# Kernel tuning notes

Hardware: AMD Instinct MI355X
Metric: run time of the kernel (lower is better)

Reference implementation:

```python
import jax, jax.numpy as jnp
import numpy as np

V, E, H, B, T = 50000, 300, 512, 256, 64
D_OUT = 3
EPS = 1e-5


def setup_inputs() -> dict:
    key = jax.random.key(0)
    ks = jax.random.split(key, 16)
    s = lambda k, shape: (jax.random.normal(k, shape, jnp.float32) * 0.05)
    return {
        "premise": jax.random.randint(ks[0], (T, B), 0, V),
        "hypothesis": jax.random.randint(ks[1], (T, B), 0, V),
        "embed": s(ks[2], (V, E)),
        "W_ih": s(ks[3], (4 * H, E)),
        "W_hh": s(ks[4], (4 * H, H)),
        "b_ih": s(ks[5], (4 * H,)),
        "b_hh": s(ks[6], (4 * H,)),
        "bn0_g": jnp.ones((4 * H,), jnp.float32),
        "bn0_b": jnp.zeros((4 * H,), jnp.float32),
        "W0": s(ks[7], (4 * H, 4 * H)),
        "b0": s(ks[8], (4 * H,)),
        "bn1_g": jnp.ones((4 * H,), jnp.float32),
        "bn1_b": jnp.zeros((4 * H,), jnp.float32),
        "W1": s(ks[9], (4 * H, 4 * H)),
        "b1": s(ks[10], (4 * H,)),
        "bno_g": jnp.ones((4 * H,), jnp.float32),
        "bno_b": jnp.zeros((4 * H,), jnp.float32),
        "Wo": s(ks[11], (D_OUT, 4 * H)),
        "bo": s(ks[12], (D_OUT,)),
    }


def _lstm_final_h(xs, W_ih, W_hh, bias):
    # xs: [T, N, E]; shared-weight LSTMCell scan, returns final hidden [N, H]
    x_proj = jnp.einsum('tne,ge->tng', xs, W_ih) + bias  # hoist input GEMM out of the recurrence
    n = xs.shape[1]
    h0 = jnp.zeros((n, H), xs.dtype)

    def step(carry, xg):
        h, c = carry
        gates = xg + h @ W_hh.T
        i, f, g, o = jnp.split(gates, 4, axis=-1)  # torch LSTMCell gate order
        c = jax.nn.sigmoid(f) * c + jax.nn.sigmoid(i) * jnp.tanh(g)
        h = jax.nn.sigmoid(o) * jnp.tanh(c)
        return (h, c), None

    (h, _), _ = jax.lax.scan(step, (h0, h0), x_proj)
    return h


def _bn(x, g, b):
    # BatchNorm1d in training mode: biased batch stats
    mu = x.mean(0)
    var = x.var(0)
    return (x - mu) * jax.lax.rsqrt(var + EPS) * g + b


def reference(premise, hypothesis, embed, W_ih, W_hh, b_ih, b_hh,
              bn0_g, bn0_b, W0, b0, bn1_g, bn1_b, W1, b1,
              bno_g, bno_b, Wo, bo):
    p = embed[premise]      # [T, B, E]
    hyp = embed[hypothesis]  # [T, B, E]
    combined = jnp.concatenate([p, hyp], axis=1)  # [T, 2B, E]
    bias = b_ih + b_hh
    h_fw = _lstm_final_h(combined, W_ih, W_hh, bias)          # forward direction
    h_bw = _lstm_final_h(combined[::-1], W_ih, W_hh, bias)    # backward direction (shared cell)
    feat = jnp.concatenate([h_fw[:B], h_bw[:B], h_fw[B:], h_bw[B:]], axis=1)  # [B, 4H]
    x = jax.nn.relu(_bn(feat, bn0_g, bn0_b) @ W0.T + b0)
    x = jax.nn.relu(_bn(x, bn1_g, bn1_b) @ W1.T + b1)
    return _bn(x, bno_g, bno_b) @ Wo.T + bo  # [B, d_out]
```

## Files before the change

### kernel.cpp

```cpp
#include <hip/hip_runtime.h>
#include <hip/hip_bf16.h>


typedef __attribute__((ext_vector_type(8))) short bf16x8;
typedef __attribute__((ext_vector_type(4))) float f32x4;
typedef __attribute__((ext_vector_type(4))) unsigned int u32x4;

#define DEVI __device__ __forceinline__

template<int N> struct IC { static constexpr int v = N; };

DEVI void async16(const void* g, void* l) {
  __builtin_amdgcn_global_load_lds((const __attribute__((address_space(1))) void*)g,
                                   (__attribute__((address_space(3))) void*)l,
                                   16, 0, 0);
}
DEVI void async16_coh(const void* g, void* l) {
  __builtin_amdgcn_global_load_lds((const __attribute__((address_space(1))) void*)g,
                                   (__attribute__((address_space(3))) void*)l,
                                   16, 0, 17);
}
DEVI void store16_coh(void* addr, u32x4 v) {
  asm volatile("global_store_dwordx4 %0, %1, off sc0 sc1" ::"v"(addr), "v"(v) : "memory");
}
DEVI bf16x8 load16_pin(const void* addr) {
  bf16x8 r;
  asm volatile("global_load_dwordx4 %0, %1, off" : "=v"(r) : "v"(addr) : "memory");
  return r;
}
template<int N> DEVI void vmwait_barrier() {
  asm volatile("s_waitcnt vmcnt(%0)" ::"i"(N) : "memory");
  __builtin_amdgcn_s_barrier();
  __builtin_amdgcn_sched_barrier(0);
}
DEVI float sigmf_(float x) { return 1.f / (1.f + __expf(-x)); }
DEVI float tanhf_(float x) {
  float a = __expf(-2.f * fabsf(x));
  float t = (1.f - a) / (1.f + a);
  return copysignf(t, x);
}
DEVI __hip_bfloat16 f2b(float x) { return __float2bfloat16(x); }
DEVI float b2f(__hip_bfloat16 x) { return __bfloat162float(x); }

__global__ void cvt_f32_bf16(const float* __restrict__ src,
                             __hip_bfloat16* __restrict__ dst, int n4) {
  int i = blockIdx.x * 256 + threadIdx.x;
  int stride = gridDim.x * 256;
  for (; i < n4; i += stride) {
    float4 v = ((const float4*)src)[i];
    union { __hip_bfloat16 h[4]; uint2 u; } o;
    o.h[0] = f2b(v.x); o.h[1] = f2b(v.y); o.h[2] = f2b(v.z); o.h[3] = f2b(v.w);
    ((uint2*)dst)[i] = o.u;
  }
}

__global__ void pack_wih(const float* __restrict__ W_ih,
                         const float* __restrict__ b_ih,
                         const float* __restrict__ b_hh,
                         __hip_bfloat16* __restrict__ WihP,
                         float* __restrict__ biasL) {
  int tid = blockIdx.x * 256 + threadIdx.x;
  int stride = gridDim.x * 256;
  for (int i = tid; i < 2048 * 320; i += stride) {
    int r = i / 320, c = i - r * 320;
    WihP[i] = (c < 300) ? f2b(W_ih[r * 300 + c]) : f2b(0.f);
  }
  if (tid < 2048) biasL[tid] = b_ih[tid] + b_hh[tid];
}

__global__ void gather_kernel(const int* __restrict__ prem, const int* __restrict__ hyp,
                              const float* __restrict__ embed,
                              __hip_bfloat16* __restrict__ Ain) {
  int row = blockIdx.x * 4 + (threadIdx.x >> 6);
  int lane = threadIdx.x & 63;
  int tt = row >> 9, n = row & 511;
  int tok = (n < 256) ? prem[tt * 256 + n] : hyp[tt * 256 + (n - 256)];
  const float4* e4 = (const float4*)(embed + (size_t)tok * 300);
  uint2* d2 = (uint2*)(Ain + (size_t)row * 320);
  for (int j = lane; j < 75; j += 64) {
    float4 v = e4[j];
    union { __hip_bfloat16 h[4]; uint2 u; } o;
    o.h[0] = f2b(v.x); o.h[1] = f2b(v.y); o.h[2] = f2b(v.z); o.h[3] = f2b(v.w);
    d2[j] = o.u;
  }
  for (int j = 75 + lane; j < 80; j += 64) d2[j] = make_uint2(0u, 0u);
}

template<int BM, int EPI>
__global__ __launch_bounds__(256)
void gemm_pipe(const __hip_bfloat16* __restrict__ A,
               const __hip_bfloat16* __restrict__ Bn,
               const float* __restrict__ bias,
               void* __restrict__ Cout, int K, int ldc) {
  constexpr int BK = 64;
  constexpr int ABYT = BM * BK * 2;
  constexpr int BBYT = 128 * BK * 2;
  constexpr int APW = BM / 32;
  constexpr int IFL = APW + 4;
  constexpr int WM = BM / 2, MT = WM / 16;
  __shared__ alignas(16) char smem[2 * ABYT + 2 * BBYT];

  const int tid = threadIdx.x, lane = tid & 63, wid = tid >> 6;
  const int wrow = wid >> 1, wcol = wid & 1;
  const int m0 = blockIdx.x * BM, n0 = blockIdx.y * 128;
  const int l8 = lane & 7, ld8 = lane >> 3;
  const int swz = (l8 ^ ld8) * 8;

  const __hip_bfloat16* Abase = A + (size_t)m0 * K;
  const __hip_bfloat16* Bbase = Bn + (size_t)n0 * K;

  f32x4 acc[MT][4];
#pragma unroll
  for (int i = 0; i < MT; ++i)
#pragma unroll
    for (int j = 0; j < 4; ++j) acc[i][j] = {0.f, 0.f, 0.f, 0.f};

  auto stage = [&](int buf, int kt) {
    const __hip_bfloat16* as = Abase + kt * BK + swz;
    char* ad = smem + buf * ABYT;
#pragma unroll
    for (int s = 0; s < APW; ++s) {
      int iss = wid * APW + s;
      async16(as + (size_t)(iss * 8 + ld8) * K, ad + iss * 1024);
    }
    const __hip_bfloat16* bs = Bbase + kt * BK + swz;
    char* bd = smem + 2 * ABYT + buf * BBYT;
#pragma unroll
    for (int s = 0; s < 4; ++s) {
      int iss = wid * 4 + s;
      async16(bs + (size_t)(iss * 8 + ld8) * K, bd + iss * 1024);
    }
  };

  const int nk = K / BK;
  stage(0, 0);
  for (int kt = 0; kt < nk; ++kt) {
    if (kt + 1 < nk) {
      stage((kt + 1) & 1, kt + 1);
      vmwait_barrier<IFL>();
    } else {
      vmwait_barrier<0>();
    }
    const __hip_bfloat16* ab = (const __hip_bfloat16*)(smem + (kt & 1) * ABYT);
    const __hip_bfloat16* bb = (const __hip_bfloat16*)(smem + 2 * ABYT + (kt & 1) * BBYT);
#pragma unroll
    for (int kk = 0; kk < BK; kk += 32) {
      bf16x8 af[MT], bf[4];
#pragma unroll
      for (int i = 0; i < MT; ++i) {
        int r = wrow * WM + i * 16 + (lane & 15);
        af[i] = *(const bf16x8*)&ab[r * BK + ((kk + (lane >> 4) * 8) ^ ((r & 7) * 8))];
      }
#pragma unroll
      for (int j = 0; j < 4; ++j) {
        int r = wcol * 64 + j * 16 + (lane & 15);
        bf[j] = *(const bf16x8*)&bb[r * BK + ((kk + (lane >> 4) * 8) ^ ((r & 7) * 8))];
      }
#pragma unroll
      for (int i = 0; i < MT; ++i)
#pragma unroll
        for (int j = 0; j < 4; ++j)
          acc[i][j] = __builtin_amdgcn_mfma_f32_16x16x32_bf16(af[i], bf[j], acc[i][j], 0, 0, 0);
    }
    __builtin_amdgcn_s_barrier();
  }

  if (EPI == 2) {
#pragma unroll
    for (int i = 0; i < MT; ++i)
#pragma unroll
      for (int j = 0; j < 4; ++j) {
        union { __hip_bfloat16 h[4]; uint2 u; } o;
#pragma unroll
        for (int rr = 0; rr < 4; ++rr) o.h[rr] = f2b(acc[i][j][rr]);
        size_t slot = (((size_t)blockIdx.x * 16 + blockIdx.y) * 4 + wid) * 16 + i * 4 + j;
        *(uint2*)((char*)Cout + slot * 512 + lane * 8) = o.u;
      }
    return;
  }

  __syncthreads();
  float* Csm = (float*)smem;
#pragma unroll
  for (int i = 0; i < MT; ++i)
#pragma unroll
    for (int j = 0; j < 4; ++j)
#pragma unroll
      for (int rr = 0; rr < 4; ++rr) {
        int row = wrow * WM + i * 16 + (lane >> 4) * 4 + rr;
        int col = wcol * 64 + j * 16 + (lane & 15);
        Csm[row * 128 + (col ^ ((row & 7) << 2))] = acc[i][j][rr];
      }
  __syncthreads();
#pragma unroll
  for (int it = 0; it < BM / 16; ++it) {
    int idx = it * 256 + tid;
    int row = idx >> 4;
    int cb = (idx & 15) * 8;
    int sw = (row & 7) << 2;
    float4 v0 = *(const float4*)&Csm[row * 128 + (cb ^ sw)];
    float4 v1 = *(const float4*)&Csm[row * 128 + ((cb + 4) ^ sw)];
    float4 b0 = *(const float4*)&bias[n0 + cb];
    float4 b1 = *(const float4*)&bias[n0 + cb + 4];
    v0.x = fmaxf(v0.x + b0.x, 0.f); v0.y = fmaxf(v0.y + b0.y, 0.f);
    v0.z = fmaxf(v0.z + b0.z, 0.f); v0.w = fmaxf(v0.w + b0.w, 0.f);
    v1.x = fmaxf(v1.x + b1.x, 0.f); v1.y = fmaxf(v1.y + b1.y, 0.f);
    v1.z = fmaxf(v1.z + b1.z, 0.f); v1.w = fmaxf(v1.w + b1.w, 0.f);
    size_t base = (size_t)(m0 + row) * ldc + n0 + cb;
    *(float4*)&((float*)Cout)[base] = v0;
    *(float4*)&((float*)Cout)[base + 4] = v1;
  }
}

__global__ __launch_bounds__(256, 1)
void lstm_persist(const __hip_bfloat16* __restrict__ xp,
                  const __hip_bfloat16* __restrict__ Whh,
                  const float* __restrict__ biasL,
                  __hip_bfloat16* __restrict__ hA,
                  __hip_bfloat16* __restrict__ hB,
                  int* __restrict__ ctr) {
  extern __shared__ char smem[];
  const int tid = threadIdx.x, lane = tid & 63, wid = tid >> 6;
  const int bid = blockIdx.x;
  const int grp = (bid & 7) | ((bid >> 7) << 3);
  const int jt = (bid >> 3) & 15;
  const int m0 = grp * 64;
  const int l8 = lane & 7, ld8 = lane >> 3;
  const int swz = (l8 ^ ld8) * 8;

  bf16x8 w[2][16];
  for (int h = 0; h < 2; ++h) {
#pragma unroll
    for (int kt = 0; kt < 8; ++kt)
#pragma unroll
      for (int s = 0; s < 2; ++s) {
        int iss = wid * 2 + s;
        int r = h * 64 + iss * 8 + ld8;
        int g = jt * 32 + (r >> 5) * 512 + (r & 31);
        async16(Whh + (size_t)g * 512 + kt * 64 + swz,
                smem + kt * 8192 + iss * 1024);
      }
    asm volatile("s_waitcnt vmcnt(0)" ::: "memory");
    __builtin_amdgcn_s_barrier();
    __builtin_amdgcn_sched_barrier(0);
    if ((wid >> 1) == h) {
      const __hip_bfloat16* wb = (const __hip_bfloat16*)smem;
      const int lw = wid & 1;
#pragma unroll
      for (int j = 0; j < 2; ++j)
#pragma unroll
        for (int ka = 0; ka < 16; ++ka) {
          int r = lw * 32 + j * 16 + (lane & 15);
          int kt = ka >> 1, kk = (ka & 1) * 32;
          w[j][ka] = *(const bf16x8*)&wb[kt * 4096 + r * 64 +
                                         ((kk + (lane >> 4) * 8) ^ ((r & 7) * 8))];
        }
    }
    __syncthreads();
  }

  const int jsel = (lane >> 5) & 1;
  const int qx = (lane >> 3) & 3;
  const int lane_x = (lane & 31) * 2;
  const int lane_lo = (lane & 7) * 2;
  const int col5b = jsel * 16 + lane_lo;
  const int wrx = grp & 1;
  const int wcx = (jt & 3) >> 1;
  const int widx = wrx * 2 + wcx;
  const int jx = (jt & 1) * 2 + jsel;
  const int ntb = jt >> 2;

  float bias_[4][2];
#pragma unroll
  for (int g = 0; g < 4; ++g)
#pragma unroll
    for (int cc = 0; cc < 2; ++cc)
      bias_[g][cc] = biasL[g * 512 + jt * 32 + col5b + cc];

  float c_[8];
#pragma unroll
  for (int e = 0; e < 8; ++e) c_[e] = 0.f;

  for (int t = 0; t < 64; ++t) {
    const __hip_bfloat16* hin = (t & 1) ? hB : hA;
    __hip_bfloat16* hout = (t & 1) ? hA : hB;

#pragma unroll
    for (int kt = 0; kt < 8; ++kt)
#pragma unroll
      for (int s = 0; s < 2; ++s) {
        int iss = wid * 2 + s;
        async16_coh(hin + (size_t)(m0 + iss * 8 + ld8) * 512 + kt * 64 + swz,
                    smem + kt * 8192 + iss * 1024);
      }
    __builtin_amdgcn_sched_barrier(0);
    const int xrow = (grp < 8) ? (t * 512 + m0) : ((63 - t) * 512 + (m0 - 512));
    const int mt2 = xrow >> 7;
    bf16x8 xg_[4];
#pragma unroll
    for (int g = 0; g < 4; ++g) {
      size_t slot = (((size_t)mt2 * 16 + g * 4 + ntb) * 4 + widx) * 16 + wid * 4 + jx;
      xg_[g] = load16_pin((const char*)xp + slot * 512 + lane_x * 8);
    }
    __builtin_amdgcn_sched_barrier(0);

    f32x4 acc[4][2];
#pragma unroll
    for (int i = 0; i < 4; ++i)
#pragma unroll
      for (int j = 0; j < 2; ++j) acc[i][j] = {0.f, 0.f, 0.f, 0.f};

    auto do_kt = [&](auto K) {
      constexpr int KT = decltype(K)::v;
      vmwait_barrier<18 - 2 * KT>();
      const __hip_bfloat16* ab = (const __hip_bfloat16*)(smem + KT * 8192);
#pragma unroll
      for (int kk = 0; kk < 64; kk += 32) {
        bf16x8 af[4];
#pragma unroll
        for (int i = 0; i < 4; ++i) {
          int r = i * 16 + (lane & 15);
          af[i] = *(const bf16x8*)&ab[r * 64 + ((kk + (lane >> 4) * 8) ^ ((r & 7) * 8))];
        }
#pragma unroll
        for (int i = 0; i < 4; ++i)
#pragma unroll
          for (int j = 0; j < 2; ++j)
            acc[i][j] = __builtin_amdgcn_mfma_f32_16x16x32_bf16(
                af[i], w[j][KT * 2 + kk / 32], acc[i][j], 0, 0, 0);
      }
    };
    do_kt(IC<0>{}); do_kt(IC<1>{}); do_kt(IC<2>{}); do_kt(IC<3>{});
    do_kt(IC<4>{}); do_kt(IC<5>{}); do_kt(IC<6>{}); do_kt(IC<7>{});

    __syncthreads();
    float* gsm = (float*)smem;
    __hip_bfloat16* hsm = (__hip_bfloat16*)(smem + 40960);
#pragma unroll
    for (int i = 0; i < 4; ++i)
#pragma unroll
      for (int j = 0; j < 2; ++j)
#pragma unroll
        for (int rr = 0; rr < 4; ++rr) {
          int row = i * 16 + (lane >> 4) * 4 + rr;
          int col = wid * 32 + j * 16 + (lane & 15);
          gsm[row * 129 + col] = acc[i][j][rr];
        }
    __syncthreads();
    asm volatile("s_waitcnt vmcnt(0)" ::: "memory");
    __builtin_amdgcn_sched_barrier(0);

    const __hip_bfloat16* x0 = (const __hip_bfloat16*)&xg_[0];
    const __hip_bfloat16* x1 = (const __hip_bfloat16*)&xg_[1];
    const __hip_bfloat16* x2 = (const __hip_bfloat16*)&xg_[2];
    const __hip_bfloat16* x3 = (const __hip_bfloat16*)&xg_[3];
#pragma unroll
    for (int cc = 0; cc < 2; ++cc) {
      int c5 = col5b + cc;
#pragma unroll
      for (int rr = 0; rr < 4; ++rr) {
        int r = wid * 16 + qx * 4 + rr;
        float gi = gsm[r * 129 + c5]      + b2f(x0[cc * 4 + rr]) + bias_[0][cc];
        float gf = gsm[r * 129 + 32 + c5] + b2f(x1[cc * 4 + rr]) + bias_[1][cc];
        float gg = gsm[r * 129 + 64 + c5] + b2f(x2[cc * 4 + rr]) + bias_[2][cc];
        float go = gsm[r * 129 + 96 + c5] + b2f(x3[cc * 4 + rr]) + bias_[3][cc];
        float cn = sigmf_(gf) * c_[cc * 4 + rr] + sigmf_(gi) * tanhf_(gg);
        float hn = sigmf_(go) * tanhf_(cn);
        c_[cc * 4 + rr] = cn;
        hsm[r * 40 + c5] = f2b(hn);
      }
    }
    __syncthreads();
    {
      int pr = tid >> 2, pj = (tid & 3) * 8;
      bf16x8 hv = *(const bf16x8*)&hsm[pr * 40 + pj];
      store16_coh(&hout[(size_t)(m0 + pr) * 512 + jt * 32 + pj], *(const u32x4*)&hv);
    }
    asm volatile("s_waitcnt vmcnt(0)" ::: "memory");
    __syncthreads();

    if (t < 63) {
      if (tid == 0) {
        const int target = 16 * (t + 1);
        int got = atomicAdd(&ctr[grp * 64], 1) + 1;
        if (got < target) {
          while (__hip_atomic_load(&ctr[grp * 64], __ATOMIC_RELAXED,
                                   __HIP_MEMORY_SCOPE_AGENT) < target)
            __builtin_amdgcn_s_sleep(1);
        }
      }
      __syncthreads();
    }
  }
}

__global__ void feat_kernel(const __hip_bfloat16* __restrict__ hA, float* __restrict__ feat) {
  int b = blockIdx.x;
  for (int c = threadIdx.x; c < 2048; c += 256) {
    int sec = c >> 9, j = c & 511;
    int row = (sec == 0) ? b : (sec == 1) ? 512 + b : (sec == 2) ? 256 + b : 768 + b;
    feat[b * 2048 + c] = b2f(hA[(size_t)row * 512 + j]);
  }
}

__global__ void bn_stats(const float* __restrict__ x, const float* __restrict__ g,
                         const float* __restrict__ b,
                         float* __restrict__ sc, float* __restrict__ sh) {
  int c = blockIdx.x * 256 + threadIdx.x;
  float s = 0.f, s2 = 0.f;
  for (int r = 0; r < 256; ++r) {
    float v = x[r * 2048 + c];
    s += v;
    s2 += v * v;
  }
  float mu = s * (1.f / 256.f);
  float var = s2 * (1.f / 256.f) - mu * mu;
  float rs = rsqrtf(var + 1e-5f);
  float scale = g[c] * rs;
  sc[c] = scale;
  sh[c] = b[c] - mu * scale;
}

__global__ void bn_apply(const float* __restrict__ x, const float* __restrict__ sc,
                         const float* __restrict__ sh, __hip_bfloat16* __restrict__ xn) {
  int i = blockIdx.x * 256 + threadIdx.x;
  int c = i & 2047;
  xn[i] = f2b(x[i] * sc[c] + sh[c]);
}

__global__ void final_kernel(const float* __restrict__ x2, const float* __restrict__ sc,
                             const float* __restrict__ sh, const float* __restrict__ Wo,
                             const float* __restrict__ bo, float* __restrict__ out) {
  __shared__ float red[3][256];
  int b = blockIdx.x, tid = threadIdx.x;
  float a0 = 0.f, a1 = 0.f, a2 = 0.f;
  for (int c = tid; c < 2048; c += 256) {
    float v = x2[b * 2048 + c] * sc[c] + sh[c];
    a0 += v * Wo[c];
    a1 += v * Wo[2048 + c];
    a2 += v * Wo[4096 + c];
  }
  red[0][tid] = a0; red[1][tid] = a1; red[2][tid] = a2;
  __syncthreads();
  for (int s = 128; s > 0; s >>= 1) {
    if (tid < s) {
      red[0][tid] += red[0][tid + s];
      red[1][tid] += red[1][tid + s];
      red[2][tid] += red[2][tid + s];
    }
    __syncthreads();
  }
  if (tid < 3) out[b * 3 + tid] = red[tid][0] + bo[tid];
}

extern "C" void kernel_launch(void* const* d_in, const int* in_sizes, int n_in,
                              void* d_out, int out_size, void* d_ws, size_t ws_size,
                              hipStream_t stream) {
  (void)in_sizes; (void)n_in; (void)out_size; (void)ws_size;
  const int* prem = (const int*)d_in[0];
  const int* hyp = (const int*)d_in[1];
  const float* embed = (const float*)d_in[2];
  const float* W_ih = (const float*)d_in[3];
  const float* W_hh = (const float*)d_in[4];
  const float* b_ih = (const float*)d_in[5];
  const float* b_hh = (const float*)d_in[6];
  const float* bn0g = (const float*)d_in[7];
  const float* bn0b = (const float*)d_in[8];
  const float* W0 = (const float*)d_in[9];
  const float* b0 = (const float*)d_in[10];
  const float* bn1g = (const float*)d_in[11];
  const float* bn1b = (const float*)d_in[12];
  const float* W1 = (const float*)d_in[13];
  const float* b1 = (const float*)d_in[14];
  const float* bnog = (const float*)d_in[15];
  const float* bnob = (const float*)d_in[16];
  const float* Wo = (const float*)d_in[17];
  const float* bo = (const float*)d_in[18];
  float* out = (float*)d_out;

  char* w = (char*)d_ws;
  size_t off = 0;
  auto alloc = [&](size_t bytes) {
    void* p = w + off;
    off += (bytes + 255) & ~(size_t)255;
    return p;
  };
  __hip_bfloat16* WihP = (__hip_bfloat16*)alloc((size_t)2048 * 320 * 2);
  __hip_bfloat16* Whhb = (__hip_bfloat16*)alloc((size_t)2048 * 512 * 2);
  __hip_bfloat16* W0b = (__hip_bfloat16*)alloc((size_t)2048 * 2048 * 2);
  __hip_bfloat16* W1b = (__hip_bfloat16*)alloc((size_t)2048 * 2048 * 2);
  float* biasL = (float*)alloc(2048 * 4);
  int* ctr = (int*)alloc(16 * 64 * 4);
  __hip_bfloat16* xp = (__hip_bfloat16*)alloc((size_t)32768 * 2048 * 2);
  size_t ain_off = off;
  __hip_bfloat16* Ain = (__hip_bfloat16*)alloc((size_t)32768 * 320 * 2);
  size_t end_off = off;
  off = ain_off;
  __hip_bfloat16* hA = (__hip_bfloat16*)alloc((size_t)1024 * 512 * 2);
  __hip_bfloat16* hB = (__hip_bfloat16*)alloc((size_t)1024 * 512 * 2);
  float* feat = (float*)alloc((size_t)256 * 2048 * 4);
  __hip_bfloat16* xn = (__hip_bfloat16*)alloc((size_t)256 * 2048 * 2);
  float* x1 = (float*)alloc((size_t)256 * 2048 * 4);
  float* x2 = (float*)alloc((size_t)256 * 2048 * 4);
  float* sc0 = (float*)alloc(2048 * 4);
  float* sh0 = (float*)alloc(2048 * 4);
  float* sc1 = (float*)alloc(2048 * 4);
  float* sh1 = (float*)alloc(2048 * 4);
  float* sc2 = (float*)alloc(2048 * 4);
  float* sh2 = (float*)alloc(2048 * 4);
  (void)end_off;

  (void)hipMemsetAsync(ctr, 0, 16 * 64 * 4, stream);
  pack_wih<<<512, 256, 0, stream>>>(W_ih, b_ih, b_hh, WihP, biasL);
  cvt_f32_bf16<<<1024, 256, 0, stream>>>(W_hh, Whhb, 2048 * 512 / 4);
  cvt_f32_bf16<<<2048, 256, 0, stream>>>(W0, W0b, 2048 * 2048 / 4);
  cvt_f32_bf16<<<2048, 256, 0, stream>>>(W1, W1b, 2048 * 2048 / 4);
  gather_kernel<<<8192, 256, 0, stream>>>(prem, hyp, embed, Ain);
  gemm_pipe<128, 2><<<dim3(256, 16), 256, 0, stream>>>(Ain, WihP, biasL, xp, 320, 2048);
  (void)hipMemsetAsync(hA, 0, (size_t)1024 * 512 * 2, stream);
  (void)hipFuncSetAttribute(reinterpret_cast<const void*>(lstm_persist),
                            hipFuncAttributeMaxDynamicSharedMemorySize, 98304);
  lstm_persist<<<256, 256, 86016, stream>>>(xp, Whhb, biasL, hA, hB, ctr);
  feat_kernel<<<256, 256, 0, stream>>>(hA, feat);
  bn_stats<<<8, 256, 0, stream>>>(feat, bn0g, bn0b, sc0, sh0);
  bn_apply<<<2048, 256, 0, stream>>>(feat, sc0, sh0, xn);
  gemm_pipe<64, 1><<<dim3(4, 16), 256, 0, stream>>>(xn, W0b, b0, x1, 2048, 2048);
  bn_stats<<<8, 256, 0, stream>>>(x1, bn1g, bn1b, sc1, sh1);
  bn_apply<<<2048, 256, 0, stream>>>(x1, sc1, sh1, xn);
  gemm_pipe<64, 1><<<dim3(4, 16), 256, 0, stream>>>(xn, W1b, b1, x2, 2048, 2048);
  bn_stats<<<8, 256, 0, stream>>>(x2, bnog, bnob, sc2, sh2);
  final_kernel<<<256, 256, 0, stream>>>(x2, sc2, sh2, Wo, bo, out);
}
```

Before: 502.1 us.

## Split persistent LSTM across 512 blocks with XCD-local fast path and pipelined loads

The persistent LSTM kernel now uses 512 blocks of 16 hidden columns each instead of 256 blocks of 32, with two blocks per CU and a smaller LDS footprint. Loading of h is now a 4-slot ring that overlaps with the MFMA work, and the LDS gate exchange uses a simpler transpose. A startup handshake checks whether every block in a row group landed on the same XCD. If so, h loads and stores skip the system-coherent cache bits. The gain is more parallelism and cheaper memory ops per step, at the cost of twice as many blocks in each group barrier and reliance on XCD placement detection.

```diff
diff --git a/kernel.cpp b/kernel.cpp
--- a/kernel.cpp
+++ b/kernel.cpp
@@ -4,29 +4,25 @@
 
 typedef __attribute__((ext_vector_type(8))) short bf16x8;
 typedef __attribute__((ext_vector_type(4))) float f32x4;
-typedef __attribute__((ext_vector_type(4))) unsigned int u32x4;
+typedef __attribute__((ext_vector_type(2))) unsigned int u32x2;
 
 #define DEVI __device__ __forceinline__
 
 template<int N> struct IC { static constexpr int v = N; };
 
-DEVI void async16(const void* g, void* l) {
+template<int AUX> DEVI void async16t(const void* g, void* l) {
   __builtin_amdgcn_global_load_lds((const __attribute__((address_space(1))) void*)g,
                                    (__attribute__((address_space(3))) void*)l,
-                                   16, 0, 0);
-}
-DEVI void async16_coh(const void* g, void* l) {
-  __builtin_amdgcn_global_load_lds((const __attribute__((address_space(1))) void*)g,
-                                   (__attribute__((address_space(3))) void*)l,
-                                   16, 0, 17);
-}
-DEVI void store16_coh(void* addr, u32x4 v) {
-  asm volatile("global_store_dwordx4 %0, %1, off sc0 sc1" ::"v"(addr), "v"(v) : "memory");
-}
-DEVI bf16x8 load16_pin(const void* addr) {
-  bf16x8 r;
-  asm volatile("global_load_dwordx4 %0, %1, off" : "=v"(r) : "v"(addr) : "memory");
+                                   16, 0, AUX);
+}
+DEVI void async16(const void* g, void* l) { async16t<0>(g, l); }
+DEVI u32x2 load8_pin(const void* addr) {
+  u32x2 r;
+  asm volatile("global_load_dwordx2 %0, %1, off" : "=v"(r) : "v"(addr) : "memory");
   return r;
+}
+DEVI void storeh_coh(void* a, unsigned int v) {
+  asm volatile("global_store_short %0, %1, off sc0 sc1" ::"v"(a), "v"(v) : "memory");
 }
 template<int N> DEVI void vmwait_barrier() {
   asm volatile("s_waitcnt vmcnt(%0)" ::"i"(N) : "memory");
@@ -212,7 +208,7 @@
   }
 }
 
-__global__ __launch_bounds__(256, 1)
+__global__ __launch_bounds__(256, 2)
 void lstm_persist(const __hip_bfloat16* __restrict__ xp,
                   const __hip_bfloat16* __restrict__ Whh,
                   const float* __restrict__ biasL,
@@ -222,176 +218,176 @@
   extern __shared__ char smem[];
   const int tid = threadIdx.x, lane = tid & 63, wid = tid >> 6;
   const int bid = blockIdx.x;
-  const int grp = (bid & 7) | ((bid >> 7) << 3);
-  const int jt = (bid >> 3) & 15;
+  const int grp = (bid & 7) | ((bid >> 8) << 3);
+  const int jt2 = (bid >> 3) & 31;
   const int m0 = grp * 64;
   const int l8 = lane & 7, ld8 = lane >> 3;
   const int swz = (l8 ^ ld8) * 8;
 
-  bf16x8 w[2][16];
-  for (int h = 0; h < 2; ++h) {
-#pragma unroll
-    for (int kt = 0; kt < 8; ++kt)
+  bf16x8 w[16];
+  for (int hh = 0; hh < 2; ++hh) {
+#pragma unroll
+    for (int kt2 = 0; kt2 < 4; ++kt2)
 #pragma unroll
       for (int s = 0; s < 2; ++s) {
         int iss = wid * 2 + s;
-        int r = h * 64 + iss * 8 + ld8;
-        int g = jt * 32 + (r >> 5) * 512 + (r & 31);
-        async16(Whh + (size_t)g * 512 + kt * 64 + swz,
-                smem + kt * 8192 + iss * 1024);
+        int r = iss * 8 + ld8;
+        int Wrow = (r >> 4) * 512 + jt2 * 16 + (r & 15);
+        async16(Whh + (size_t)Wrow * 512 + (hh * 4 + kt2) * 64 + swz,
+                smem + kt2 * 8192 + iss * 1024);
       }
     asm volatile("s_waitcnt vmcnt(0)" ::: "memory");
     __builtin_amdgcn_s_barrier();
     __builtin_amdgcn_sched_barrier(0);
-    if ((wid >> 1) == h) {
+    {
       const __hip_bfloat16* wb = (const __hip_bfloat16*)smem;
-      const int lw = wid & 1;
-#pragma unroll
-      for (int j = 0; j < 2; ++j)
-#pragma unroll
-        for (int ka = 0; ka < 16; ++ka) {
-          int r = lw * 32 + j * 16 + (lane & 15);
-          int kt = ka >> 1, kk = (ka & 1) * 32;
-          w[j][ka] = *(const bf16x8*)&wb[kt * 4096 + r * 64 +
-                                         ((kk + (lane >> 4) * 8) ^ ((r & 7) * 8))];
+      int r = wid * 16 + (lane & 15);
+#pragma unroll
+      for (int kt2 = 0; kt2 < 4; ++kt2)
+#pragma unroll
+        for (int kkh = 0; kkh < 2; ++kkh)
+          w[(hh * 4 + kt2) * 2 + kkh] =
+              *(const bf16x8*)&wb[kt2 * 4096 + r * 64 +
+                                  ((kkh * 32 + (lane >> 4) * 8) ^ ((r & 7) * 8))];
+    }
+    __syncthreads();
+  }
+
+  int* flag = (int*)(smem + 49152);
+  if (tid == 0) {
+    int xcd = (int)(__builtin_amdgcn_s_getreg((31 << 11) | 20) & 15);
+    int o1 = atomicOr(&ctr[grp * 64 + 1], 1 << xcd);
+    int o2 = atomicOr(&ctr[1025], 1 << xcd);
+    asm volatile("" ::"v"(o1), "v"(o2));
+    atomicAdd(&ctr[1024], 1);
+    while (__hip_atomic_load(&ctr[1024], __ATOMIC_RELAXED, __HIP_MEMORY_SCOPE_AGENT) < 512)
+      __builtin_amdgcn_s_sleep(2);
+    int gm = __hip_atomic_load(&ctr[grp * 64 + 1], __ATOMIC_RELAXED, __HIP_MEMORY_SCOPE_AGENT);
+    int am = __hip_atomic_load(&ctr[1025], __ATOMIC_RELAXED, __HIP_MEMORY_SCOPE_AGENT);
+    *flag = (__popc((unsigned)gm) == 1 && __popc((unsigned)am) == 8) ? 1 : 0;
+  }
+  __syncthreads();
+  const bool fastpath = (*flag != 0);
+  __syncthreads();
+
+  const int q = lane >> 4, c = lane & 15;
+  const int widx = (grp & 1) * 2 + ((jt2 & 7) >> 2);
+  const int jx = jt2 & 3;
+  const int byb = jt2 >> 3;
+  float bias_[4];
+#pragma unroll
+  for (int g = 0; g < 4; ++g) bias_[g] = biasL[g * 512 + jt2 * 16 + c];
+
+  float c_[4];
+#pragma unroll
+  for (int e = 0; e < 4; ++e) c_[e] = 0.f;
+
+  auto run = [&](auto FC) {
+    constexpr bool FAST = decltype(FC)::v;
+    constexpr int AUX = FAST ? 1 : 17;
+    for (int t = 0; t < 64; ++t) {
+      const __hip_bfloat16* hin = (t & 1) ? hB : hA;
+      __hip_bfloat16* hout = (t & 1) ? hA : hB;
+
+      auto issueA = [&](int kt) {
+#pragma unroll
+        for (int s = 0; s < 2; ++s) {
+          int iss = wid * 2 + s;
+          async16t<AUX>(hin + (size_t)(m0 + iss * 8 + ld8) * 512 + kt * 64 + swz,
+                        smem + (kt & 3) * 8192 + iss * 1024);
         }
-    }
-    __syncthreads();
-  }
-
-  const int jsel = (lane >> 5) & 1;
-  const int qx = (lane >> 3) & 3;
-  const int lane_x = (lane & 31) * 2;
-  const int lane_lo = (lane & 7) * 2;
-  const int col5b = jsel * 16 + lane_lo;
-  const int wrx = grp & 1;
-  const int wcx = (jt & 3) >> 1;
-  const int widx = wrx * 2 + wcx;
-  const int jx = (jt & 1) * 2 + jsel;
-  const int ntb = jt >> 2;
-
-  float bias_[4][2];
-#pragma unroll
-  for (int g = 0; g < 4; ++g)
-#pragma unroll
-    for (int cc = 0; cc < 2; ++cc)
-      bias_[g][cc] = biasL[g * 512 + jt * 32 + col5b + cc];
-
-  float c_[8];
-#pragma unroll
-  for (int e = 0; e < 8; ++e) c_[e] = 0.f;
-
-  for (int t = 0; t < 64; ++t) {
-    const __hip_bfloat16* hin = (t & 1) ? hB : hA;
-    __hip_bfloat16* hout = (t & 1) ? hA : hB;
-
-#pragma unroll
-    for (int kt = 0; kt < 8; ++kt)
-#pragma unroll
-      for (int s = 0; s < 2; ++s) {
-        int iss = wid * 2 + s;
-        async16_coh(hin + (size_t)(m0 + iss * 8 + ld8) * 512 + kt * 64 + swz,
-                    smem + kt * 8192 + iss * 1024);
-      }
-    __builtin_amdgcn_sched_barrier(0);
-    const int xrow = (grp < 8) ? (t * 512 + m0) : ((63 - t) * 512 + (m0 - 512));
-    const int mt2 = xrow >> 7;
-    bf16x8 xg_[4];
-#pragma unroll
-    for (int g = 0; g < 4; ++g) {
-      size_t slot = (((size_t)mt2 * 16 + g * 4 + ntb) * 4 + widx) * 16 + wid * 4 + jx;
-      xg_[g] = load16_pin((const char*)xp + slot * 512 + lane_x * 8);
-    }
-    __builtin_amdgcn_sched_barrier(0);
-
-    f32x4 acc[4][2];
-#pragma unroll
-    for (int i = 0; i < 4; ++i)
-#pragma unroll
-      for (int j = 0; j < 2; ++j) acc[i][j] = {0.f, 0.f, 0.f, 0.f};
-
-    auto do_kt = [&](auto K) {
-      constexpr int KT = decltype(K)::v;
-      vmwait_barrier<18 - 2 * KT>();
-      const __hip_bfloat16* ab = (const __hip_bfloat16*)(smem + KT * 8192);
-#pragma unroll
-      for (int kk = 0; kk < 64; kk += 32) {
-        bf16x8 af[4];
-#pragma unroll
-        for (int i = 0; i < 4; ++i) {
-          int r = i * 16 + (lane & 15);
-          af[i] = *(const bf16x8*)&ab[r * 64 + ((kk + (lane >> 4) * 8) ^ ((r & 7) * 8))];
+      };
+      issueA(0); issueA(1); issueA(2);
+      __builtin_amdgcn_sched_barrier(0);
+      const int xbase = (grp < 8) ? (t * 512 + m0) : ((63 - t) * 512 + (m0 - 512));
+      const int bx = xbase >> 7;
+      u32x2 xg[4];
+#pragma unroll
+      for (int g = 0; g < 4; ++g) {
+        size_t slot = (((size_t)bx * 16 + g * 4 + byb) * 4 + widx) * 16 + wid * 4 + jx;
+        xg[g] = load8_pin((const char*)xp + slot * 512 + lane * 8);
+      }
+      __builtin_amdgcn_sched_barrier(0);
+
+      f32x4 acc[4];
+#pragma unroll
+      for (int i = 0; i < 4; ++i) acc[i] = {0.f, 0.f, 0.f, 0.f};
+
+      auto do_kt = [&](auto K) {
+        constexpr int KT = decltype(K)::v;
+        constexpr int WT[8] = {8, 8, 8, 4, 4, 4, 2, 0};
+        vmwait_barrier<WT[KT]>();
+        if constexpr (KT < 5) issueA(KT + 3);
+        const __hip_bfloat16* ab = (const __hip_bfloat16*)(smem + (KT & 3) * 8192);
+#pragma unroll
+        for (int kk = 0; kk < 64; kk += 32) {
+          bf16x8 af[4];
+#pragma unroll
+          for (int i = 0; i < 4; ++i) {
+            int r = i * 16 + (lane & 15);
+            af[i] = *(const bf16x8*)&ab[r * 64 + ((kk + (lane >> 4) * 8) ^ ((r & 7) * 8))];
+          }
+#pragma unroll
+          for (int i = 0; i < 4; ++i)
+            acc[i] = __builtin_amdgcn_mfma_f32_16x16x32_bf16(
+                af[i], w[KT * 2 + kk / 32], acc[i], 0, 0, 0);
         }
-#pragma unroll
-        for (int i = 0; i < 4; ++i)
-#pragma unroll
-          for (int j = 0; j < 2; ++j)
-            acc[i][j] = __builtin_amdgcn_mfma_f32_16x16x32_bf16(
-                af[i], w[j][KT * 2 + kk / 32], acc[i][j], 0, 0, 0);
-      }
-    };
-    do_kt(IC<0>{}); do_kt(IC<1>{}); do_kt(IC<2>{}); do_kt(IC<3>{});
-    do_kt(IC<4>{}); do_kt(IC<5>{}); do_kt(IC<6>{}); do_kt(IC<7>{});
-
-    __syncthreads();
-    float* gsm = (float*)smem;
-    __hip_bfloat16* hsm = (__hip_bfloat16*)(smem + 40960);
-#pragma unroll
-    for (int i = 0; i < 4; ++i)
-#pragma unroll
-      for (int j = 0; j < 2; ++j)
-#pragma unroll
-        for (int rr = 0; rr < 4; ++rr) {
-          int row = i * 16 + (lane >> 4) * 4 + rr;
-          int col = wid * 32 + j * 16 + (lane & 15);
-          gsm[row * 129 + col] = acc[i][j][rr];
+      };
+      do_kt(IC<0>{}); do_kt(IC<1>{}); do_kt(IC<2>{}); do_kt(IC<3>{});
+      do_kt(IC<4>{}); do_kt(IC<5>{}); do_kt(IC<6>{}); do_kt(IC<7>{});
+
+      float* gsm = (float*)(smem + 32768);
+#pragma unroll
+      for (int i = 0; i < 4; ++i)
+        *(f32x4*)(gsm + (wid * 4 + i) * 256 + lane * 4) = acc[i];
+      __syncthreads();
+      f32x4 gq[4];
+#pragma unroll
+      for (int g = 0; g < 4; ++g)
+        gq[g] = *(const f32x4*)(gsm + (g * 4 + wid) * 256 + lane * 4);
+      asm volatile("s_waitcnt vmcnt(0)" ::: "memory");
+      __builtin_amdgcn_sched_barrier(0);
+
+      union { u32x2 v; __hip_bfloat16 h[4]; } X[4];
+#pragma unroll
+      for (int g = 0; g < 4; ++g) X[g].v = xg[g];
+      __hip_bfloat16* hbase = hout + (size_t)(m0 + wid * 16 + q * 4) * 512 + jt2 * 16 + c;
+#pragma unroll
+      for (int rr = 0; rr < 4; ++rr) {
+        float gi = gq[0][rr] + b2f(X[0].h[rr]) + bias_[0];
+        float gf = gq[1][rr] + b2f(X[1].h[rr]) + bias_[1];
+        float gg = gq[2][rr] + b2f(X[2].h[rr]) + bias_[2];
+        float go = gq[3][rr] + b2f(X[3].h[rr]) + bias_[3];
+        float cn = sigmf_(gf) * c_[rr] + sigmf_(gi) * tanhf_(gg);
+        float hn = sigmf_(go) * tanhf_(cn);
+        c_[rr] = cn;
+        union { __hip_bfloat16 b; unsigned short u; } hb;
+        hb.b = f2b(hn);
+        if constexpr (FAST) {
+          hbase[rr * 512] = hb.b;
+        } else {
+          storeh_coh(hbase + rr * 512, (unsigned int)hb.u);
         }
-    __syncthreads();
-    asm volatile("s_waitcnt vmcnt(0)" ::: "memory");
-    __builtin_amdgcn_sched_barrier(0);
-
-    const __hip_bfloat16* x0 = (const __hip_bfloat16*)&xg_[0];
-    const __hip_bfloat16* x1 = (const __hip_bfloat16*)&xg_[1];
-    const __hip_bfloat16* x2 = (const __hip_bfloat16*)&xg_[2];
-    const __hip_bfloat16* x3 = (const __hip_bfloat16*)&xg_[3];
-#pragma unroll
-    for (int cc = 0; cc < 2; ++cc) {
-      int c5 = col5b + cc;
-#pragma unroll
-      for (int rr = 0; rr < 4; ++rr) {
-        int r = wid * 16 + qx * 4 + rr;
-        float gi = gsm[r * 129 + c5]      + b2f(x0[cc * 4 + rr]) + bias_[0][cc];
-        float gf = gsm[r * 129 + 32 + c5] + b2f(x1[cc * 4 + rr]) + bias_[1][cc];
-        float gg = gsm[r * 129 + 64 + c5] + b2f(x2[cc * 4 + rr]) + bias_[2][cc];
-        float go = gsm[r * 129 + 96 + c5] + b2f(x3[cc * 4 + rr]) + bias_[3][cc];
-        float cn = sigmf_(gf) * c_[cc * 4 + rr] + sigmf_(gi) * tanhf_(gg);
-        float hn = sigmf_(go) * tanhf_(cn);
-        c_[cc * 4 + rr] = cn;
-        hsm[r * 40 + c5] = f2b(hn);
-      }
-    }
-    __syncthreads();
-    {
-      int pr = tid >> 2, pj = (tid & 3) * 8;
-      bf16x8 hv = *(const bf16x8*)&hsm[pr * 40 + pj];
-      store16_coh(&hout[(size_t)(m0 + pr) * 512 + jt * 32 + pj], *(const u32x4*)&hv);
-    }
-    asm volatile("s_waitcnt vmcnt(0)" ::: "memory");
-    __syncthreads();
-
-    if (t < 63) {
-      if (tid == 0) {
-        const int target = 16 * (t + 1);
-        int got = atomicAdd(&ctr[grp * 64], 1) + 1;
-        if (got < target) {
-          while (__hip_atomic_load(&ctr[grp * 64], __ATOMIC_RELAXED,
-                                   __HIP_MEMORY_SCOPE_AGENT) < target)
-            __builtin_amdgcn_s_sleep(1);
+      }
+      asm volatile("s_waitcnt vmcnt(0)" ::: "memory");
+      __syncthreads();
+
+      if (t < 63) {
+        if (tid == 0) {
+          const int target = 32 * (t + 1);
+          int got = atomicAdd(&ctr[grp * 64], 1) + 1;
+          if (got < target) {
+            while (__hip_atomic_load(&ctr[grp * 64], __ATOMIC_RELAXED,
+                                     __HIP_MEMORY_SCOPE_AGENT) < target)
+              __builtin_amdgcn_s_sleep(1);
+          }
         }
-      }
-      __syncthreads();
-    }
-  }
+        __syncthreads();
+      }
+    }
+  };
+  if (fastpath) run(IC<1>{});
+  else          run(IC<0>{});
 }
 
 __global__ void feat_kernel(const __hip_bfloat16* __restrict__ hA, float* __restrict__ feat) {
@@ -490,7 +486,7 @@
   __hip_bfloat16* W0b = (__hip_bfloat16*)alloc((size_t)2048 * 2048 * 2);
   __hip_bfloat16* W1b = (__hip_bfloat16*)alloc((size_t)2048 * 2048 * 2);
   float* biasL = (float*)alloc(2048 * 4);
-  int* ctr = (int*)alloc(16 * 64 * 4);
+  int* ctr = (int*)alloc(2048 * 4);
   __hip_bfloat16* xp = (__hip_bfloat16*)alloc((size_t)32768 * 2048 * 2);
   size_t ain_off = off;
   __hip_bfloat16* Ain = (__hip_bfloat16*)alloc((size_t)32768 * 320 * 2);
@@ -510,7 +506,7 @@
   float* sh2 = (float*)alloc(2048 * 4);
   (void)end_off;
 
-  (void)hipMemsetAsync(ctr, 0, 16 * 64 * 4, stream);
+  (void)hipMemsetAsync(ctr, 0, 2048 * 4, stream);
   pack_wih<<<512, 256, 0, stream>>>(W_ih, b_ih, b_hh, WihP, biasL);
   cvt_f32_bf16<<<1024, 256, 0, stream>>>(W_hh, Whhb, 2048 * 512 / 4);
   cvt_f32_bf16<<<2048, 256, 0, stream>>>(W0, W0b, 2048 * 2048 / 4);
@@ -519,8 +515,8 @@
   gemm_pipe<128, 2><<<dim3(256, 16), 256, 0, stream>>>(Ain, WihP, biasL, xp, 320, 2048);
   (void)hipMemsetAsync(hA, 0, (size_t)1024 * 512 * 2, stream);
   (void)hipFuncSetAttribute(reinterpret_cast<const void*>(lstm_persist),
-                            hipFuncAttributeMaxDynamicSharedMemorySize, 98304);
-  lstm_persist<<<256, 256, 86016, stream>>>(xp, Whhb, biasL, hA, hB, ctr);
+                            hipFuncAttributeMaxDynamicSharedMemorySize, 65536);
+  lstm_persist<<<512, 256, 49408, stream>>>(xp, Whhb, biasL, hA, hB, ctr);
   feat_kernel<<<256, 256, 0, stream>>>(hA, feat);
   bn_stats<<<8, 256, 0, stream>>>(feat, bn0g, bn0b, sc0, sh0);
   bn_apply<<<2048, 256, 0, stream>>>(feat, sc0, sh0, xn);
```

Result: faster. 471.6 us (-6.1%).
